# Optimization experiments

Hardware: AMD Instinct MI355X
Metric: run time of the kernel (lower is better)

Reference implementation:

```python
import jax, jax.numpy as jnp
import numpy as np

B, N_P, N_S, N_REL, N_HIS, N_INST = 2, 2000, 48, 8192, 4, 8
N = N_P + N_S
NF = 128           # nf_particle = nf_relation = nf_effect
IN_DIM = 19        # n_his*3 + attr(2) + physics(1) + action(3) + density(1)
REL_DIM = 56       # 2*19 + 2*2 + 1 + 3*4 + 1
PSTEP = 3
MOTION_CLAMP = 100.0


def _lin(key, din, dout):
    return (jax.random.normal(key, (din, dout), jnp.float32) * 0.02,
            jnp.zeros((dout,), jnp.float32))


def setup_inputs() -> dict:
    key = jax.random.key(0)
    ks = jax.random.split(key, 20)
    # one-hot receiver/sender matrices (dense stand-in for sparse edges)
    rr_idx = jax.random.randint(ks[0], (B, N_REL), 0, N)
    rs_idx = jax.random.randint(ks[1], (B, N_REL), 0, N)
    Rr = jax.nn.one_hot(rr_idx, N, dtype=jnp.float32)  # [B, n_rel, N]
    Rs = jax.nn.one_hot(rs_idx, N, dtype=jnp.float32)
    inst_idx = jax.random.randint(ks[2], (B, N_P), 0, N_INST)
    p_instance = jax.nn.one_hot(inst_idx, N_INST, dtype=jnp.float32)  # [B, n_p, n_inst]

    inp = {
        'state': jax.random.normal(ks[3], (B, N_HIS, N, 3), jnp.float32),
        'attrs': jax.random.normal(ks[4], (B, N, 2), jnp.float32),
        'Rr': Rr, 'Rs': Rs, 'p_instance': p_instance,
        'action': jax.random.normal(ks[5], (B, N, 3), jnp.float32),
        'particle_den': jax.random.uniform(ks[6], (B,), jnp.float32),
        'physics_param': jax.random.normal(ks[7], (B, 1), jnp.float32),
    }
    inp['pe_W0'], inp['pe_b0'] = _lin(ks[8], IN_DIM, NF)
    inp['pe_W1'], inp['pe_b1'] = _lin(ks[9], NF, NF)
    inp['pe_W2'], inp['pe_b2'] = _lin(ks[10], NF, NF)
    # relation encoder
    inp['re_W0'], inp['re_b0'] = _lin(ks[11], REL_DIM, NF)
    inp['re_W1'], inp['re_b1'] = _lin(ks[12], NF, NF)
    inp['re_W2'], inp['re_b2'] = _lin(ks[13], NF, NF)
    # propagators (single Linear each)
    inp['pp_W'], inp['pp_b'] = _lin(ks[14], 2 * NF, NF)
    inp['rp_W'], inp['rp_b'] = _lin(ks[15], 3 * NF, NF)
    # non-rigid predictor (Linear-ReLU-Linear-ReLU-Linear)
    inp['np_W0'], inp['np_b0'] = _lin(ks[16], NF, NF)
    inp['np_W1'], inp['np_b1'] = _lin(ks[17], NF, NF)
    inp['np_W2'], inp['np_b2'] = _lin(ks[18], NF, 3)
    return inp


def _enc(x, W0, b0, W1, b1, W2, b2):
    x = jax.nn.relu(x @ W0 + b0)
    x = jax.nn.relu(x @ W1 + b1)
    return jax.nn.relu(x @ W2 + b2)


def reference(state, attrs, Rr, Rs, p_instance, action, particle_den, physics_param,
              pe_W0, pe_b0, pe_W1, pe_b1, pe_W2, pe_b2,
              re_W0, re_b0, re_W1, re_b1, re_W2, re_b2,
              pp_W, pp_b, rp_W, rp_b,
              np_W0, np_b0, np_W1, np_b1, np_W2, np_b2):
    b, n = attrs.shape[0], attrs.shape[1]
    n_p = p_instance.shape[1]
    n_s = n - n_p
    n_inst = p_instance.shape[2]

    # temporal residuals + current state (state_normalize=False)
    state_res = state[:, 1:] - state[:, :-1]                 # [B, n_his-1, N, 3]
    state_norm = jnp.concatenate([state_res, state[:, -1:]], axis=1)
    state_norm_t = jnp.transpose(state_norm, (0, 2, 1, 3)).reshape(b, n, N_HIS * 3)

    # particle inputs: attrs | state | physics | action | density
    phys = jnp.broadcast_to(physics_param[:, None, :], (b, n_p, physics_param.shape[1]))
    phys = jnp.concatenate([phys, jnp.zeros((b, n_s, physics_param.shape[1]), state.dtype)], axis=1)
    den = jnp.broadcast_to(particle_den[:, None, None], (b, n_p, 1))
    den = jnp.concatenate([den, jnp.zeros((b, n_s, 1), state.dtype)], axis=1)
    p_inputs = jnp.concatenate([attrs, state_norm_t, phys, action, den], axis=2)  # [B,N,19]

    # relation inputs via one-hot gather (dense bmm in original)
    p_r = jnp.matmul(Rr, p_inputs)
    p_s = jnp.matmul(Rs, p_inputs)
    a_r = jnp.matmul(Rr, attrs)
    a_s = jnp.matmul(Rs, attrs)
    g = jnp.concatenate([p_instance, jnp.zeros((b, n_s, n_inst), state.dtype)], axis=1)
    group_diff = jnp.sum(jnp.abs(jnp.matmul(Rr, g) - jnp.matmul(Rs, g)), axis=2, keepdims=True)
    pos_diff = jnp.matmul(Rr, state_norm_t) - jnp.matmul(Rs, state_norm_t)
    dens_diff = jnp.matmul(Rr, den) - jnp.matmul(Rs, den)
    rel_inputs = jnp.concatenate([p_r, p_s, a_r, a_s, group_diff, pos_diff, dens_diff], axis=2)  # [B,n_rel,56]

    particle_encode = _enc(p_inputs, pe_W0, pe_b0, pe_W1, pe_b1, pe_W2, pe_b2)   # [B,N,128]
    relation_encode = _enc(rel_inputs, re_W0, re_b0, re_W1, re_b1, re_W2, re_b2)  # [B,n_rel,128]

    particle_effect = particle_encode
    for _ in range(PSTEP):
        eff_r = jnp.matmul(Rr, particle_effect)   # gather to edges
        eff_s = jnp.matmul(Rs, particle_effect)
        rel_in = jnp.concatenate([relation_encode, eff_r, eff_s], axis=2)   # [B,n_rel,384]
        effect_rel = jax.nn.relu(rel_in @ rp_W + rp_b)                      # relation propagator
        agg = jnp.einsum('brn,brd->bnd', Rr, effect_rel)                    # scatter-add (Rr_t bmm)
        p_in = jnp.concatenate([particle_encode, agg], axis=2)              # [B,N,256]
        particle_effect = jax.nn.relu(p_in @ pp_W + pp_b + particle_effect)  # residual propagator

    h = jax.nn.relu(particle_effect[:, :n_p] @ np_W0 + np_b0)
    h = jax.nn.relu(h @ np_W1 + np_b1)
    motion = h @ np_W2 + np_b2                                              # [B,n_p,3]
    motion = jnp.clip(motion, -MOTION_CLAMP, MOTION_CLAMP)
    pred_pos = state[:, -1, :n_p] + motion
    return pred_pos
```

## Files before the change

### kernel.cpp

```cpp
#include <hip/hip_runtime.h>

#define B 2
#define N_P 2000
#define N_ALL 2048
#define N_REL 8192
#define N_INST 8
#define NF 128
#define DEG_CAP 64

typedef unsigned short u16;
typedef __attribute__((ext_vector_type(8))) short bf16x8;
typedef __attribute__((ext_vector_type(4))) float f32x4;

__device__ __forceinline__ u16 f2bf(float f) {
    union { float f; unsigned u; } v; v.f = f;
    unsigned r = v.u + 0x7FFFu + ((v.u >> 16) & 1u);
    return (u16)(r >> 16);
}
__device__ __forceinline__ float bf2f(u16 h) {
    union { unsigned u; float f; } v; v.u = ((unsigned)h) << 16; return v.f;
}

#define MFMA16(a, b, c) __builtin_amdgcn_mfma_f32_16x16x32_bf16((a), (b), (c), 0, 0, 0)
#define SWZ(row, col) ((col) ^ (((row) & 7) << 3))

#define NWT 13
struct WtCvt {
    const float* src[NWT];
    int K[NWT];
    int Kpad[NWT];
    int cum[NWT + 1];
};

#define H0_SCAN_BLKS 8192
#define H0_CVT_BLKS  752
#define H0_PIN_BLKS  16
#define H0_TOTAL (H0_SCAN_BLKS + H0_CVT_BLKS + H0_PIN_BLKS)

__global__ __launch_bounds__(256) void scan_h0(
    const float* __restrict__ Rr, const float* __restrict__ Rs,
    int* __restrict__ rr, int* __restrict__ rs,
    WtCvt d, u16* __restrict__ wt, int wt_total,
    const float* __restrict__ state, const float* __restrict__ attrs,
    const float* __restrict__ action, const float* __restrict__ den,
    const float* __restrict__ phys, u16* __restrict__ P)
{
    int blk = blockIdx.x;
    if (blk < H0_SCAN_BLKS) {
        int lane = threadIdx.x & 63;
        int r = blk * 4 + (threadIdx.x >> 6);
        const float* base = (r < 16384 ? Rr + (size_t)r * N_ALL
                                       : Rs + (size_t)(r - 16384) * N_ALL);
        const f32x4* s = reinterpret_cast<const f32x4*>(base) + lane;
        f32x4 v[4];
        #pragma unroll
        for (int i = 0; i < 4; ++i) v[i] = s[64 * i];
        int f = -1;
        #pragma unroll
        for (int i = 0; i < 4; ++i) {
            int bi = (lane + 64 * i) * 4;
            if (v[i].x != 0.f) f = bi;
            if (v[i].y != 0.f) f = bi + 1;
            if (v[i].z != 0.f) f = bi + 2;
            if (v[i].w != 0.f) f = bi + 3;
        }
        #pragma unroll
        for (int off = 32; off; off >>= 1) f = max(f, __shfl_xor(f, off));
        if (lane == 0) {
            int* outp = (r < 16384) ? rr : rs;
            outp[r & 16383] = f;
        }
        return;
    }
    blk -= H0_SCAN_BLKS;
    if (blk < H0_CVT_BLKS) {
        int t = blk * 256 + threadIdx.x;
        if (t >= wt_total) return;
        int m = 0;
        while (t >= d.cum[m + 1]) m++;
        int loc = t - d.cum[m];
        int Kp = d.Kpad[m];
        int c = loc / Kp, k = loc - c * Kp;
        float v = (k < d.K[m]) ? d.src[m][(size_t)k * NF + c] : 0.f;
        wt[t] = f2bf(v);
        return;
    }
    blk -= H0_CVT_BLKS;
    {
        int t = blk * 256 + threadIdx.x;
        if (t >= B * N_ALL) return;
        int b = t >> 11, n = t & 2047;
        float o[19];
        o[0] = attrs[t * 2]; o[1] = attrs[t * 2 + 1];
        #pragma unroll
        for (int h = 0; h < 3; ++h)
            #pragma unroll
            for (int c = 0; c < 3; ++c)
                o[2 + h * 3 + c] = state[(((size_t)b * 4 + h + 1) * N_ALL + n) * 3 + c]
                                 - state[(((size_t)b * 4 + h)     * N_ALL + n) * 3 + c];
        #pragma unroll
        for (int c = 0; c < 3; ++c)
            o[11 + c] = state[(((size_t)b * 4 + 3) * N_ALL + n) * 3 + c];
        o[14] = (n < N_P) ? phys[b] : 0.f;
        #pragma unroll
        for (int c = 0; c < 3; ++c) o[15 + c] = action[t * 3 + c];
        o[18] = (n < N_P) ? den[b] : 0.f;
        u16* dst = P + (size_t)t * 32;
        #pragma unroll
        for (int k = 0; k < 19; ++k) dst[k] = f2bf(o[k]);
        #pragma unroll
        for (int k = 19; k < 32; ++k) dst[k] = 0;
    }
}

template<int START>
__global__ __launch_bounds__(256) void scan_stripe(
    const float* __restrict__ Rr, const float* __restrict__ Rs,
    int* __restrict__ rr, int* __restrict__ rs, int* __restrict__ cnt)
{
    if (blockIdx.x >= 8192) {
        int t = (blockIdx.x - 8192) * 256 + threadIdx.x;
        if (t < B * N_ALL) cnt[t] = 0;
        return;
    }
    int lane = threadIdx.x & 63;
    int r = blockIdx.x * 4 + (threadIdx.x >> 6);
    int* outp = (r < 16384) ? rr : rs;
    int e = r & 16383;
    if (outp[e] >= 0) return;
    const float* base = ((r < 16384) ? Rr + (size_t)r * N_ALL
                                     : Rs + (size_t)(r - 16384) * N_ALL) + START;
    const f32x4* s = reinterpret_cast<const f32x4*>(base + lane * 8);
    f32x4 v0 = s[0], v1 = s[1];
    int f = -1;
    int bi = START + lane * 8;
    #pragma unroll
    for (int j = 0; j < 4; ++j) {
        if (v0[j] != 0.f) f = bi + j;
        if (v1[j] != 0.f) f = bi + 4 + j;
    }
    #pragma unroll
    for (int off = 32; off; off >>= 1) f = max(f, __shfl_xor(f, off));
    if (lane == 0) outp[e] = f;
}

__device__ __forceinline__ void ldsA_gemm(const u16* T, const u16* __restrict__ wtm,
                                          f32x4 acc[8], int r16, int g4)
{
    #pragma unroll
    for (int cf = 0; cf < 8; ++cf) acc[cf] = (f32x4){0.f, 0.f, 0.f, 0.f};
    #pragma unroll
    for (int kf = 0; kf < 4; ++kf) {
        int kcol = kf * 32 + g4 * 8;
        bf16x8 a = *reinterpret_cast<const bf16x8*>(&T[r16 * NF + SWZ(r16, kcol)]);
        #pragma unroll
        for (int cf = 0; cf < 8; ++cf) {
            bf16x8 bv = *reinterpret_cast<const bf16x8*>(wtm + (size_t)(cf * 16 + r16) * NF + kcol);
            acc[cf] = MFMA16(a, bv, acc[cf]);
        }
    }
}
__device__ __forceinline__ void tile_store(u16* T, f32x4 acc[8], const float* __restrict__ bias,
                                           int r16, int g4)
{
    #pragma unroll
    for (int cf = 0; cf < 8; ++cf) {
        float bb = bias[cf * 16 + r16];
        #pragma unroll
        for (int i = 0; i < 4; ++i) {
            int row = g4 * 4 + i, col = cf * 16 + r16;
            T[row * NF + SWZ(row, col)] = f2bf(fmaxf(acc[cf][i] + bb, 0.f));
        }
    }
}

#define ENC_REL_BLKS 256
#define ENC_PART_BLKS 64
#define ENC_FILL_BLKS 8
#define ENC_TOTAL (ENC_REL_BLKS + ENC_PART_BLKS + ENC_FILL_BLKS)

__global__ __launch_bounds__(256) void enc2(
    const u16* __restrict__ P, const float* __restrict__ attrs,
    const float* __restrict__ p_inst,
    const int* __restrict__ rr, const int* __restrict__ rs,
    const u16* __restrict__ wpe0, const u16* __restrict__ wpe1, const u16* __restrict__ wpe2,
    const float* __restrict__ pb0, const float* __restrict__ pb1, const float* __restrict__ pb2,
    const u16* __restrict__ wre0, const u16* __restrict__ wre1, const u16* __restrict__ wre2,
    const float* __restrict__ rb0, const float* __restrict__ rb1, const float* __restrict__ rb2,
    const float* __restrict__ rp_b, const u16* __restrict__ wrp0t,
    const u16* __restrict__ wpp0t, const u16* __restrict__ wrp1t, const u16* __restrict__ wrp2t,
    u16* __restrict__ penc, u16* __restrict__ relencW,
    float* __restrict__ Zp, u16* __restrict__ Zrs0,
    int* __restrict__ cnt, int2* __restrict__ buckets)
{
    __shared__ __align__(16) char smem[40960];
    int tid = threadIdx.x;
    int blk = blockIdx.x;

    if (blk >= ENC_REL_BLKS + ENC_PART_BLKS) {
        int t = (blk - ENC_REL_BLKS - ENC_PART_BLKS) * 256 + tid;
        for (int e = t; e < B * N_REL; e += ENC_FILL_BLKS * 256) {
            int n = ((e >> 13) << 11) + rr[e];
            int pos = atomicAdd(&cnt[n], 1);
            if (pos < DEG_CAP) {
                int2 v; v.x = e; v.y = ((e >> 13) << 11) + rs[e];
                buckets[(size_t)n * DEG_CAP + pos] = v;
            }
        }
        return;
    }

    u16* ri = (u16*)smem;
    int w = tid >> 6, lane = tid & 63;
    int r16 = lane & 15, g4 = lane >> 4;
    u16* T0 = (u16*)(smem + 8192 + w * 8192);
    u16* T1 = T0 + 2048;
    f32x4 acc[8];

    if (blk < ENC_REL_BLKS) {
        {
            int row = tid >> 2;
            int q = tid & 3;
            int grow = blk * 64 + row;
            int b = grow >> 13;
            int ir = rr[grow], is_ = rs[grow];
            const u16* pr = P + ((size_t)(b << 11) + ir) * 32;
            const u16* ps = P + ((size_t)(b << 11) + is_) * 32;
            float gd = 0.f;
            if (q == 2) {
                #pragma unroll
                for (int k = 0; k < N_INST; ++k) {
                    float gr = (ir < N_P) ? p_inst[((size_t)b * N_P + ir) * N_INST + k] : 0.f;
                    float gs = (is_ < N_P) ? p_inst[((size_t)b * N_P + is_) * N_INST + k] : 0.f;
                    gd += fabsf(gr - gs);
                }
            }
            #pragma unroll
            for (int j = 0; j < 16; ++j) {
                int c = q * 16 + j;
                u16 hv;
                if (c < 19)       hv = pr[c];
                else if (c < 38)  hv = ps[c - 19];
                else if (c < 40)  hv = f2bf(attrs[((size_t)(b << 11) + ir) * 2 + (c - 38)]);
                else if (c < 42)  hv = f2bf(attrs[((size_t)(b << 11) + is_) * 2 + (c - 40)]);
                else if (c == 42) hv = f2bf(gd);
                else if (c < 55)  hv = f2bf(bf2f(pr[c - 41]) - bf2f(ps[c - 41]));
                else if (c == 55) hv = f2bf(bf2f(pr[18]) - bf2f(ps[18]));
                else              hv = 0;
                ri[row * 64 + SWZ(row, c)] = hv;
            }
        }
        __syncthreads();
        int rbase = blk * 64 + w * 16;
        #pragma unroll
        for (int cf = 0; cf < 8; ++cf) acc[cf] = (f32x4){0.f, 0.f, 0.f, 0.f};
        #pragma unroll
        for (int kf = 0; kf < 2; ++kf) {
            int kcol = kf * 32 + g4 * 8;
            int lr = w * 16 + r16;
            bf16x8 a = *reinterpret_cast<const bf16x8*>(&ri[lr * 64 + SWZ(lr, kcol)]);
            #pragma unroll
            for (int cf = 0; cf < 8; ++cf) {
                bf16x8 bv = *reinterpret_cast<const bf16x8*>(wre0 + (size_t)(cf * 16 + r16) * 64 + kcol);
                acc[cf] = MFMA16(a, bv, acc[cf]);
            }
        }
        tile_store(T0, acc, rb0, r16, g4);
        ldsA_gemm(T0, wre1, acc, r16, g4);
        tile_store(T1, acc, rb1, r16, g4);
        ldsA_gemm(T1, wre2, acc, r16, g4);
        tile_store(T0, acc, rb2, r16, g4);
        ldsA_gemm(T0, wrp0t, acc, r16, g4);
        #pragma unroll
        for (int cf = 0; cf < 8; ++cf) {
            float bb = rp_b[cf * 16 + r16];
            #pragma unroll
            for (int i = 0; i < 4; ++i) {
                int grow = rbase + g4 * 4 + i;
                relencW[(size_t)grow * NF + cf * 16 + r16] = f2bf(acc[cf][i] + bb);
            }
        }
        return;
    }

    int blk2 = blk - ENC_REL_BLKS;
    int rbase = blk2 * 64 + w * 16;
    #pragma unroll
    for (int cf = 0; cf < 8; ++cf) acc[cf] = (f32x4){0.f, 0.f, 0.f, 0.f};
    {
        int kcol = g4 * 8;
        bf16x8 a = *reinterpret_cast<const bf16x8*>(P + (size_t)(rbase + r16) * 32 + kcol);
        #pragma unroll
        for (int cf = 0; cf < 8; ++cf) {
            bf16x8 bv = *reinterpret_cast<const bf16x8*>(wpe0 + (size_t)(cf * 16 + r16) * 32 + kcol);
            acc[cf] = MFMA16(a, bv, acc[cf]);
        }
    }
    tile_store(T0, acc, pb0, r16, g4);
    ldsA_gemm(T0, wpe1, acc, r16, g4);
    tile_store(T1, acc, pb1, r16, g4);
    ldsA_gemm(T1, wpe2, acc, r16, g4);
    tile_store(T0, acc, pb2, r16, g4);
    #pragma unroll
    for (int cf = 0; cf < 8; ++cf)
        #pragma unroll
        for (int i = 0; i < 4; ++i) {
            int row = g4 * 4 + i, col = cf * 16 + r16;
            penc[(size_t)(rbase + row) * NF + col] = T0[row * NF + SWZ(row, col)];
        }
    ldsA_gemm(T0, wpp0t, acc, r16, g4);
    #pragma unroll
    for (int cf = 0; cf < 8; ++cf)
        #pragma unroll
        for (int i = 0; i < 4; ++i)
            Zp[(size_t)(rbase + g4 * 4 + i) * NF + cf * 16 + r16] = acc[cf][i];
    ldsA_gemm(T0, wrp1t, acc, r16, g4);
    #pragma unroll
    for (int cf = 0; cf < 8; ++cf)
        #pragma unroll
        for (int i = 0; i < 4; ++i)
            Zrs0[(size_t)(rbase + g4 * 4 + i) * 256 + cf * 16 + r16] = f2bf(acc[cf][i]);
    ldsA_gemm(T0, wrp2t, acc, r16, g4);
    #pragma unroll
    for (int cf = 0; cf < 8; ++cf)
        #pragma unroll
        for (int i = 0; i < 4; ++i)
            Zrs0[(size_t)(rbase + g4 * 4 + i) * 256 + 128 + cf * 16 + r16] = f2bf(acc[cf][i]);
}

template<int LAST>
__global__ __launch_bounds__(256) void step_c(
    const int* __restrict__ cnt, const int2* __restrict__ buckets,
    const u16* __restrict__ relencW, const u16* __restrict__ Zrs,
    const float* __restrict__ Zp, const float* __restrict__ pp_b,
    const u16* __restrict__ eff_prev,
    const u16* __restrict__ wpp1t, const u16* __restrict__ wrp1t, const u16* __restrict__ wrp2t,
    u16* __restrict__ eff_out, u16* __restrict__ Zrs_out,
    const u16* __restrict__ wnp0t, const u16* __restrict__ wnp1t,
    const float* __restrict__ nb0, const float* __restrict__ nb1,
    const float* __restrict__ np_W2, const float* __restrict__ nb2,
    const float* __restrict__ state, float* __restrict__ out)
{
    __shared__ float aggL[32][NF];
    __shared__ u16 tw[2][2][16 * NF];
    int w = threadIdx.x >> 6, lane = threadIdx.x & 63;
    int r16 = lane & 15, g4 = lane >> 4;
    int nbase = blockIdx.x * 32;

    {
        int ln = threadIdx.x >> 3;
        int q  = threadIdx.x & 7;
        int n  = nbase + ln;
        const u16* zrp = Zrs + (size_t)n * 256 + q * 16;
        bf16x8 z0 = *reinterpret_cast<const bf16x8*>(zrp);
        bf16x8 z1 = *reinterpret_cast<const bf16x8*>(zrp + 8);
        float zr[16];
        #pragma unroll
        for (int j = 0; j < 8; ++j) { zr[j] = bf2f((u16)z0[j]); zr[8 + j] = bf2f((u16)z1[j]); }
        float a16[16];
        #pragma unroll
        for (int j = 0; j < 16; ++j) a16[j] = 0.f;
        int k1 = min(cnt[n], DEG_CAP);
        const int2* eb_base = buckets + (size_t)n * DEG_CAP;
        for (int k = 0; k < k1; k += 4) {
            int m = k1 - k;
            int2 eb[4];
            #pragma unroll
            for (int t = 0; t < 4; ++t) if (t < m) eb[t] = eb_base[k + t];
            #pragma unroll
            for (int t = 0; t < 4; ++t) if (t < m) {
                const u16* rwp = relencW + (size_t)eb[t].x * NF + q * 16;
                const u16* zsp = Zrs + (size_t)eb[t].y * 256 + 128 + q * 16;
                bf16x8 rw0 = *reinterpret_cast<const bf16x8*>(rwp);
                bf16x8 rw1 = *reinterpret_cast<const bf16x8*>(rwp + 8);
                bf16x8 zs0 = *reinterpret_cast<const bf16x8*>(zsp);
                bf16x8 zs1 = *reinterpret_cast<const bf16x8*>(zsp + 8);
                #pragma unroll
                for (int j = 0; j < 8; ++j) {
                    a16[j]     += fmaxf(bf2f((u16)rw0[j]) + zr[j]     + bf2f((u16)zs0[j]), 0.f);
                    a16[8 + j] += fmaxf(bf2f((u16)rw1[j]) + zr[8 + j] + bf2f((u16)zs1[j]), 0.f);
                }
            }
        }
        int c0 = q * 16;
        int pc0 = c0 ^ ((ln & 7) << 3);
        int pc1 = (c0 + 8) ^ ((ln & 7) << 3);
        #pragma unroll
        for (int j = 0; j < 8; ++j) {
            aggL[ln][pc0 + j] = a16[j];
            aggL[ln][pc1 + j] = a16[8 + j];
        }
    }
    __syncthreads();
    if (w >= 2) return;

    u16* T0 = tw[w][0]; u16* T1 = tw[w][1];
    f32x4 acc[8];
    #pragma unroll
    for (int cf = 0; cf < 8; ++cf) acc[cf] = (f32x4){0.f, 0.f, 0.f, 0.f};
    int lrow = w * 16 + r16;
    #pragma unroll
    for (int kf = 0; kf < 4; ++kf) {
        int kcol = kf * 32 + g4 * 8;
        int pc = kcol ^ ((lrow & 7) << 3);
        float4 lo = *reinterpret_cast<const float4*>(&aggL[lrow][pc]);
        float4 hi = *reinterpret_cast<const float4*>(&aggL[lrow][pc + 4]);
        bf16x8 a;
        a[0] = (short)f2bf(lo.x); a[1] = (short)f2bf(lo.y);
        a[2] = (short)f2bf(lo.z); a[3] = (short)f2bf(lo.w);
        a[4] = (short)f2bf(hi.x); a[5] = (short)f2bf(hi.y);
        a[6] = (short)f2bf(hi.z); a[7] = (short)f2bf(hi.w);
        #pragma unroll
        for (int cf = 0; cf < 8; ++cf) {
            bf16x8 bv = *reinterpret_cast<const bf16x8*>(wpp1t + (size_t)(cf * 16 + r16) * NF + kcol);
            acc[cf] = MFMA16(a, bv, acc[cf]);
        }
    }
    int rbase = nbase + w * 16;
    #pragma unroll
    for (int cf = 0; cf < 8; ++cf) {
        int col = cf * 16 + r16;
        float bb = pp_b[col];
        #pragma unroll
        for (int i = 0; i < 4; ++i) {
            int trow = g4 * 4 + i;
            int grow = rbase + trow;
            float v = acc[cf][i] + bb + Zp[(size_t)grow * NF + col]
                    + bf2f(eff_prev[(size_t)grow * NF + col]);
            u16 hv = f2bf(fmaxf(v, 0.f));
            T0[trow * NF + SWZ(trow, col)] = hv;
            if (!LAST) eff_out[(size_t)grow * NF + col] = hv;
        }
    }
    if (!LAST) {
        ldsA_gemm(T0, wrp1t, acc, r16, g4);
        #pragma unroll
        for (int cf = 0; cf < 8; ++cf)
            #pragma unroll
            for (int i = 0; i < 4; ++i)
                Zrs_out[(size_t)(rbase + g4 * 4 + i) * 256 + cf * 16 + r16] = f2bf(acc[cf][i]);
        ldsA_gemm(T0, wrp2t, acc, r16, g4);
        #pragma unroll
        for (int cf = 0; cf < 8; ++cf)
            #pragma unroll
            for (int i = 0; i < 4; ++i)
                Zrs_out[(size_t)(rbase + g4 * 4 + i) * 256 + 128 + cf * 16 + r16] = f2bf(acc[cf][i]);
    } else {
        ldsA_gemm(T0, wnp0t, acc, r16, g4);
        tile_store(T1, acc, nb0, r16, g4);
        ldsA_gemm(T1, wnp1t, acc, r16, g4);
        tile_store(T0, acc, nb1, r16, g4);
        if (g4 < 3) {
            int grow = rbase + r16;
            int b = grow >> 11, n = grow & 2047;
            if (n < N_P) {
                float s = nb2[g4];
                for (int k = 0; k < NF; ++k)
                    s += bf2f(T0[r16 * NF + SWZ(r16, k)]) * np_W2[k * 3 + g4];
                s = fminf(fmaxf(s, -100.f), 100.f);
                out[((size_t)b * N_P + n) * 3 + g4] =
                    s + state[(((size_t)b * 4 + 3) * N_ALL + n) * 3 + g4];
            }
        }
    }
}

extern "C" void kernel_launch(void* const* d_in, const int* in_sizes, int n_in,
                              void* d_out, int out_size, void* d_ws, size_t ws_size,
                              hipStream_t stream) {
    (void)in_sizes; (void)n_in; (void)out_size; (void)ws_size;
    const float* state      = (const float*)d_in[0];
    const float* attrs      = (const float*)d_in[1];
    const float* Rr         = (const float*)d_in[2];
    const float* Rs         = (const float*)d_in[3];
    const float* p_instance = (const float*)d_in[4];
    const float* action     = (const float*)d_in[5];
    const float* den        = (const float*)d_in[6];
    const float* phys       = (const float*)d_in[7];
    const float* pe_W0 = (const float*)d_in[8];  const float* pe_b0 = (const float*)d_in[9];
    const float* pe_W1 = (const float*)d_in[10]; const float* pe_b1 = (const float*)d_in[11];
    const float* pe_W2 = (const float*)d_in[12]; const float* pe_b2 = (const float*)d_in[13];
    const float* re_W0 = (const float*)d_in[14]; const float* re_b0 = (const float*)d_in[15];
    const float* re_W1 = (const float*)d_in[16]; const float* re_b1 = (const float*)d_in[17];
    const float* re_W2 = (const float*)d_in[18]; const float* re_b2 = (const float*)d_in[19];
    const float* pp_W  = (const float*)d_in[20]; const float* pp_b  = (const float*)d_in[21];
    const float* rp_W  = (const float*)d_in[22]; const float* rp_b  = (const float*)d_in[23];
    const float* np_W0 = (const float*)d_in[24]; const float* np_b0 = (const float*)d_in[25];
    const float* np_W1 = (const float*)d_in[26]; const float* np_b1 = (const float*)d_in[27];
    const float* np_W2 = (const float*)d_in[28]; const float* np_b2 = (const float*)d_in[29];

    char* base = (char*)d_ws;
    size_t off = 0;
    auto alloc = [&](size_t bytes) -> void* {
        off = (off + 255) & ~(size_t)255;
        void* p = base + off; off += bytes; return p;
    };
    const int RN = B * N_ALL;
    const int RE = B * N_REL;
    int*   rr      = (int*)alloc(RE * 4);
    int*   rs      = (int*)alloc(RE * 4);
    int*   cnt     = (int*)alloc(RN * 4);
    int2*  buckets = (int2*)alloc((size_t)RN * DEG_CAP * 8);
    u16*   P       = (u16*)alloc((size_t)RN * 32 * 2);
    u16*   penc    = (u16*)alloc((size_t)RN * NF * 2);
    u16*   relencW = (u16*)alloc((size_t)RE * NF * 2);
    float* Zp      = (float*)alloc((size_t)RN * NF * 4);
    u16*   ZrsA    = (u16*)alloc((size_t)RN * 256 * 2);
    u16*   ZrsB    = (u16*)alloc((size_t)RN * 256 * 2);
    u16*   effX    = (u16*)alloc((size_t)RN * NF * 2);
    u16*   effY    = (u16*)alloc((size_t)RN * NF * 2);

    WtCvt d;
    const float* srcs[NWT] = {pe_W0, pe_W1, pe_W2, re_W0, re_W1, re_W2,
                              rp_W, rp_W + 128 * NF, rp_W + 256 * NF,
                              pp_W, pp_W + 128 * NF, np_W0, np_W1};
    const int Ks[NWT]  = {19, 128, 128, 56, 128, 128, 128, 128, 128, 128, 128, 128, 128};
    const int Kps[NWT] = {32, 128, 128, 64, 128, 128, 128, 128, 128, 128, 128, 128, 128};
    d.cum[0] = 0;
    for (int i = 0; i < NWT; ++i) {
        d.src[i] = srcs[i]; d.K[i] = Ks[i]; d.Kpad[i] = Kps[i];
        d.cum[i + 1] = d.cum[i] + NF * Kps[i];
    }
    int wt_total = d.cum[NWT];
    u16* wt = (u16*)alloc((size_t)wt_total * 2);
    const u16 *wpe0 = wt + d.cum[0], *wpe1 = wt + d.cum[1], *wpe2 = wt + d.cum[2];
    const u16 *wre0 = wt + d.cum[3], *wre1 = wt + d.cum[4], *wre2 = wt + d.cum[5];
    const u16 *wrp0t = wt + d.cum[6], *wrp1t = wt + d.cum[7], *wrp2t = wt + d.cum[8];
    const u16 *wpp0t = wt + d.cum[9], *wpp1t = wt + d.cum[10];
    const u16 *wnp0t = wt + d.cum[11], *wnp1t = wt + d.cum[12];

    scan_h0<<<H0_TOTAL, 256, 0, stream>>>(Rr, Rs, rr, rs, d, wt, wt_total,
                                          state, attrs, action, den, phys, P);
    scan_stripe<1024><<<8192, 256, 0, stream>>>(Rr, Rs, rr, rs, cnt);
    scan_stripe<1536><<<8192 + 16, 256, 0, stream>>>(Rr, Rs, rr, rs, cnt);

    enc2<<<ENC_TOTAL, 256, 0, stream>>>(P, attrs, p_instance, rr, rs,
        wpe0, wpe1, wpe2, pe_b0, pe_b1, pe_b2,
        wre0, wre1, wre2, re_b0, re_b1, re_b2,
        rp_b, wrp0t, wpp0t, wrp1t, wrp2t,
        penc, relencW, Zp, ZrsA, cnt, buckets);

    const u16* Zcur = ZrsA;
    const u16* effp = penc;
    u16* Znext[2] = {ZrsB, ZrsA};
    u16* effn[2]  = {effX, effY};
    for (int s = 0; s < 3; ++s) {
        if (s < 2) {
            step_c<0><<<RN / 32, 256, 0, stream>>>(cnt, buckets, relencW, Zcur,
                Zp, pp_b, effp, wpp1t, wrp1t, wrp2t, effn[s], Znext[s],
                wnp0t, wnp1t, np_b0, np_b1, np_W2, np_b2, state, (float*)d_out);
            Zcur = Znext[s];
            effp = effn[s];
        } else {
            step_c<1><<<RN / 32, 256, 0, stream>>>(cnt, buckets, relencW, Zcur,
                Zp, pp_b, effp, wpp1t, wrp1t, wrp2t, nullptr, nullptr,
                wnp0t, wnp1t, np_b0, np_b1, np_W2, np_b2, state, (float*)d_out);
        }
    }
}
```

Before: 130.5 us.

## Fuse three propagation step launches into one persistent kernel with grid barriers

The three step_c launches are replaced by a single step_m kernel of 128 blocks that runs all three propagation steps, separated by a software grid barrier built from an atomic counter. The counter is reset inside scan_stripe. The aim is to remove two kernel launch gaps and their tail effects. The risk is that the spin barrier needs all 128 blocks resident at once, which holds on this GPU; block-to-node mapping is unchanged (RN/32 = 128).

```diff
diff --git a/kernel.cpp b/kernel.cpp
--- a/kernel.cpp
+++ b/kernel.cpp
@@ -116,11 +116,13 @@
 template<int START>
 __global__ __launch_bounds__(256) void scan_stripe(
     const float* __restrict__ Rr, const float* __restrict__ Rs,
-    int* __restrict__ rr, int* __restrict__ rs, int* __restrict__ cnt)
+    int* __restrict__ rr, int* __restrict__ rs,
+    int* __restrict__ cnt, int* __restrict__ bar)
 {
     if (blockIdx.x >= 8192) {
         int t = (blockIdx.x - 8192) * 256 + threadIdx.x;
         if (t < B * N_ALL) cnt[t] = 0;
+        if (t == 0) *bar = 0;
         return;
     }
     int lane = threadIdx.x & 63;
@@ -328,21 +330,35 @@
             Zrs0[(size_t)(rbase + g4 * 4 + i) * 256 + 128 + cf * 16 + r16] = f2bf(acc[cf][i]);
 }
 
+struct StepP {
+    const int* cnt; const int2* buckets;
+    const u16* relencW; const float* Zp; const float* pp_b;
+    const u16* wpp1t; const u16* wrp1t; const u16* wrp2t;
+    const u16 *wnp0t, *wnp1t; const float *nb0, *nb1;
+    const float* np_W2; const float* nb2;
+    const float* state; float* out;
+    const u16* penc; u16 *effX, *effY, *ZrsA, *ZrsB;
+    int* bar;
+};
+
+__device__ __forceinline__ void grid_bar(int* bar, int expected)
+{
+    __syncthreads();
+    if (threadIdx.x == 0) {
+        __threadfence();
+        atomicAdd(bar, 1);
+        while (atomicAdd(bar, 0) < expected) { }
+        __threadfence();
+    }
+    __syncthreads();
+}
+
 template<int LAST>
-__global__ __launch_bounds__(256) void step_c(
-    const int* __restrict__ cnt, const int2* __restrict__ buckets,
-    const u16* __restrict__ relencW, const u16* __restrict__ Zrs,
-    const float* __restrict__ Zp, const float* __restrict__ pp_b,
-    const u16* __restrict__ eff_prev,
-    const u16* __restrict__ wpp1t, const u16* __restrict__ wrp1t, const u16* __restrict__ wrp2t,
-    u16* __restrict__ eff_out, u16* __restrict__ Zrs_out,
-    const u16* __restrict__ wnp0t, const u16* __restrict__ wnp1t,
-    const float* __restrict__ nb0, const float* __restrict__ nb1,
-    const float* __restrict__ np_W2, const float* __restrict__ nb2,
-    const float* __restrict__ state, float* __restrict__ out)
-{
-    __shared__ float aggL[32][NF];
-    __shared__ u16 tw[2][2][16 * NF];
+__device__ void step_body(const StepP& p,
+                          float (*aggL)[NF], u16* twbase,
+                          const u16* Zrs, const u16* eff_prev,
+                          u16* eff_out, u16* Zrs_out)
+{
     int w = threadIdx.x >> 6, lane = threadIdx.x & 63;
     int r16 = lane & 15, g4 = lane >> 4;
     int nbase = blockIdx.x * 32;
@@ -360,8 +376,8 @@
         float a16[16];
         #pragma unroll
         for (int j = 0; j < 16; ++j) a16[j] = 0.f;
-        int k1 = min(cnt[n], DEG_CAP);
-        const int2* eb_base = buckets + (size_t)n * DEG_CAP;
+        int k1 = min(p.cnt[n], DEG_CAP);
+        const int2* eb_base = p.buckets + (size_t)n * DEG_CAP;
         for (int k = 0; k < k1; k += 4) {
             int m = k1 - k;
             int2 eb[4];
@@ -369,7 +385,7 @@
             for (int t = 0; t < 4; ++t) if (t < m) eb[t] = eb_base[k + t];
             #pragma unroll
             for (int t = 0; t < 4; ++t) if (t < m) {
-                const u16* rwp = relencW + (size_t)eb[t].x * NF + q * 16;
+                const u16* rwp = p.relencW + (size_t)eb[t].x * NF + q * 16;
                 const u16* zsp = Zrs + (size_t)eb[t].y * 256 + 128 + q * 16;
                 bf16x8 rw0 = *reinterpret_cast<const bf16x8*>(rwp);
                 bf16x8 rw1 = *reinterpret_cast<const bf16x8*>(rwp + 8);
@@ -392,77 +408,93 @@
         }
     }
     __syncthreads();
-    if (w >= 2) return;
-
-    u16* T0 = tw[w][0]; u16* T1 = tw[w][1];
-    f32x4 acc[8];
-    #pragma unroll
-    for (int cf = 0; cf < 8; ++cf) acc[cf] = (f32x4){0.f, 0.f, 0.f, 0.f};
-    int lrow = w * 16 + r16;
-    #pragma unroll
-    for (int kf = 0; kf < 4; ++kf) {
-        int kcol = kf * 32 + g4 * 8;
-        int pc = kcol ^ ((lrow & 7) << 3);
-        float4 lo = *reinterpret_cast<const float4*>(&aggL[lrow][pc]);
-        float4 hi = *reinterpret_cast<const float4*>(&aggL[lrow][pc + 4]);
-        bf16x8 a;
-        a[0] = (short)f2bf(lo.x); a[1] = (short)f2bf(lo.y);
-        a[2] = (short)f2bf(lo.z); a[3] = (short)f2bf(lo.w);
-        a[4] = (short)f2bf(hi.x); a[5] = (short)f2bf(hi.y);
-        a[6] = (short)f2bf(hi.z); a[7] = (short)f2bf(hi.w);
+    if (w < 2) {
+        u16* T0 = twbase + w * 4096;
+        u16* T1 = T0 + 2048;
+        f32x4 acc[8];
+        #pragma unroll
+        for (int cf = 0; cf < 8; ++cf) acc[cf] = (f32x4){0.f, 0.f, 0.f, 0.f};
+        int lrow = w * 16 + r16;
+        #pragma unroll
+        for (int kf = 0; kf < 4; ++kf) {
+            int kcol = kf * 32 + g4 * 8;
+            int pc = kcol ^ ((lrow & 7) << 3);
+            float4 lo = *reinterpret_cast<const float4*>(&aggL[lrow][pc]);
+            float4 hi = *reinterpret_cast<const float4*>(&aggL[lrow][pc + 4]);
+            bf16x8 a;
+            a[0] = (short)f2bf(lo.x); a[1] = (short)f2bf(lo.y);
+            a[2] = (short)f2bf(lo.z); a[3] = (short)f2bf(lo.w);
+            a[4] = (short)f2bf(hi.x); a[5] = (short)f2bf(hi.y);
+            a[6] = (short)f2bf(hi.z); a[7] = (short)f2bf(hi.w);
+            #pragma unroll
+            for (int cf = 0; cf < 8; ++cf) {
+                bf16x8 bv = *reinterpret_cast<const bf16x8*>(p.wpp1t + (size_t)(cf * 16 + r16) * NF + kcol);
+                acc[cf] = MFMA16(a, bv, acc[cf]);
+            }
+        }
+        int rbase = nbase + w * 16;
         #pragma unroll
         for (int cf = 0; cf < 8; ++cf) {
-            bf16x8 bv = *reinterpret_cast<const bf16x8*>(wpp1t + (size_t)(cf * 16 + r16) * NF + kcol);
-            acc[cf] = MFMA16(a, bv, acc[cf]);
-        }
-    }
-    int rbase = nbase + w * 16;
-    #pragma unroll
-    for (int cf = 0; cf < 8; ++cf) {
-        int col = cf * 16 + r16;
-        float bb = pp_b[col];
-        #pragma unroll
-        for (int i = 0; i < 4; ++i) {
-            int trow = g4 * 4 + i;
-            int grow = rbase + trow;
-            float v = acc[cf][i] + bb + Zp[(size_t)grow * NF + col]
-                    + bf2f(eff_prev[(size_t)grow * NF + col]);
-            u16 hv = f2bf(fmaxf(v, 0.f));
-            T0[trow * NF + SWZ(trow, col)] = hv;
-            if (!LAST) eff_out[(size_t)grow * NF + col] = hv;
-        }
-    }
-    if (!LAST) {
-        ldsA_gemm(T0, wrp1t, acc, r16, g4);
-        #pragma unroll
-        for (int cf = 0; cf < 8; ++cf)
-            #pragma unroll
-            for (int i = 0; i < 4; ++i)
-                Zrs_out[(size_t)(rbase + g4 * 4 + i) * 256 + cf * 16 + r16] = f2bf(acc[cf][i]);
-        ldsA_gemm(T0, wrp2t, acc, r16, g4);
-        #pragma unroll
-        for (int cf = 0; cf < 8; ++cf)
-            #pragma unroll
-            for (int i = 0; i < 4; ++i)
-                Zrs_out[(size_t)(rbase + g4 * 4 + i) * 256 + 128 + cf * 16 + r16] = f2bf(acc[cf][i]);
-    } else {
-        ldsA_gemm(T0, wnp0t, acc, r16, g4);
-        tile_store(T1, acc, nb0, r16, g4);
-        ldsA_gemm(T1, wnp1t, acc, r16, g4);
-        tile_store(T0, acc, nb1, r16, g4);
-        if (g4 < 3) {
-            int grow = rbase + r16;
-            int b = grow >> 11, n = grow & 2047;
-            if (n < N_P) {
-                float s = nb2[g4];
-                for (int k = 0; k < NF; ++k)
-                    s += bf2f(T0[r16 * NF + SWZ(r16, k)]) * np_W2[k * 3 + g4];
-                s = fminf(fmaxf(s, -100.f), 100.f);
-                out[((size_t)b * N_P + n) * 3 + g4] =
-                    s + state[(((size_t)b * 4 + 3) * N_ALL + n) * 3 + g4];
-            }
-        }
-    }
+            int col = cf * 16 + r16;
+            float bb = p.pp_b[col];
+            #pragma unroll
+            for (int i = 0; i < 4; ++i) {
+                int trow = g4 * 4 + i;
+                int grow = rbase + trow;
+                float v = acc[cf][i] + bb + p.Zp[(size_t)grow * NF + col]
+                        + bf2f(eff_prev[(size_t)grow * NF + col]);
+                u16 hv = f2bf(fmaxf(v, 0.f));
+                T0[trow * NF + SWZ(trow, col)] = hv;
+                if (!LAST) eff_out[(size_t)grow * NF + col] = hv;
+            }
+        }
+        if (!LAST) {
+            f32x4 acc2[8];
+            ldsA_gemm(T0, p.wrp1t, acc2, r16, g4);
+            #pragma unroll
+            for (int cf = 0; cf < 8; ++cf)
+                #pragma unroll
+                for (int i = 0; i < 4; ++i)
+                    Zrs_out[(size_t)(rbase + g4 * 4 + i) * 256 + cf * 16 + r16] = f2bf(acc2[cf][i]);
+            ldsA_gemm(T0, p.wrp2t, acc2, r16, g4);
+            #pragma unroll
+            for (int cf = 0; cf < 8; ++cf)
+                #pragma unroll
+                for (int i = 0; i < 4; ++i)
+                    Zrs_out[(size_t)(rbase + g4 * 4 + i) * 256 + 128 + cf * 16 + r16] = f2bf(acc2[cf][i]);
+        } else {
+            f32x4 acc2[8];
+            ldsA_gemm(T0, p.wnp0t, acc2, r16, g4);
+            tile_store(T1, acc2, p.nb0, r16, g4);
+            ldsA_gemm(T1, p.wnp1t, acc2, r16, g4);
+            tile_store(T0, acc2, p.nb1, r16, g4);
+            if (g4 < 3) {
+                int grow = rbase + r16;
+                int b = grow >> 11, n = grow & 2047;
+                if (n < N_P) {
+                    float s = p.nb2[g4];
+                    for (int k = 0; k < NF; ++k)
+                        s += bf2f(T0[r16 * NF + SWZ(r16, k)]) * p.np_W2[k * 3 + g4];
+                    s = fminf(fmaxf(s, -100.f), 100.f);
+                    p.out[((size_t)b * N_P + n) * 3 + g4] =
+                        s + p.state[(((size_t)b * 4 + 3) * N_ALL + n) * 3 + g4];
+                }
+            }
+        }
+    }
+}
+
+__global__ __launch_bounds__(256) void step_m(StepP p)
+{
+    __shared__ float aggL[32][NF];
+    __shared__ u16 tw[2][2][16 * NF];
+    u16* twbase = &tw[0][0][0];
+
+    step_body<0>(p, aggL, twbase, p.ZrsA, p.penc, p.effX, p.ZrsB);
+    grid_bar(p.bar, 128);
+    step_body<0>(p, aggL, twbase, p.ZrsB, p.effX, p.effY, p.ZrsA);
+    grid_bar(p.bar, 256);
+    step_body<1>(p, aggL, twbase, p.ZrsA, p.effY, nullptr, nullptr);
 }
 
 extern "C" void kernel_launch(void* const* d_in, const int* in_sizes, int n_in,
@@ -500,6 +532,7 @@
     int*   rr      = (int*)alloc(RE * 4);
     int*   rs      = (int*)alloc(RE * 4);
     int*   cnt     = (int*)alloc(RN * 4);
+    int*   bar     = (int*)alloc(256);
     int2*  buckets = (int2*)alloc((size_t)RN * DEG_CAP * 8);
     u16*   P       = (u16*)alloc((size_t)RN * 32 * 2);
     u16*   penc    = (u16*)alloc((size_t)RN * NF * 2);
@@ -531,8 +564,8 @@
 
     scan_h0<<<H0_TOTAL, 256, 0, stream>>>(Rr, Rs, rr, rs, d, wt, wt_total,
                                           state, attrs, action, den, phys, P);
-    scan_stripe<1024><<<8192, 256, 0, stream>>>(Rr, Rs, rr, rs, cnt);
-    scan_stripe<1536><<<8192 + 16, 256, 0, stream>>>(Rr, Rs, rr, rs, cnt);
+    scan_stripe<1024><<<8192, 256, 0, stream>>>(Rr, Rs, rr, rs, cnt, bar);
+    scan_stripe<1536><<<8192 + 16, 256, 0, stream>>>(Rr, Rs, rr, rs, cnt, bar);
 
     enc2<<<ENC_TOTAL, 256, 0, stream>>>(P, attrs, p_instance, rr, rs,
         wpe0, wpe1, wpe2, pe_b0, pe_b1, pe_b2,
@@ -540,21 +573,15 @@
         rp_b, wrp0t, wpp0t, wrp1t, wrp2t,
         penc, relencW, Zp, ZrsA, cnt, buckets);
 
-    const u16* Zcur = ZrsA;
-    const u16* effp = penc;
-    u16* Znext[2] = {ZrsB, ZrsA};
-    u16* effn[2]  = {effX, effY};
-    for (int s = 0; s < 3; ++s) {
-        if (s < 2) {
-            step_c<0><<<RN / 32, 256, 0, stream>>>(cnt, buckets, relencW, Zcur,
-                Zp, pp_b, effp, wpp1t, wrp1t, wrp2t, effn[s], Znext[s],
-                wnp0t, wnp1t, np_b0, np_b1, np_W2, np_b2, state, (float*)d_out);
-            Zcur = Znext[s];
-            effp = effn[s];
-        } else {
-            step_c<1><<<RN / 32, 256, 0, stream>>>(cnt, buckets, relencW, Zcur,
-                Zp, pp_b, effp, wpp1t, wrp1t, wrp2t, nullptr, nullptr,
-                wnp0t, wnp1t, np_b0, np_b1, np_W2, np_b2, state, (float*)d_out);
-        }
-    }
-}
+    StepP sp;
+    sp.cnt = cnt; sp.buckets = buckets;
+    sp.relencW = relencW; sp.Zp = Zp; sp.pp_b = pp_b;
+    sp.wpp1t = wpp1t; sp.wrp1t = wrp1t; sp.wrp2t = wrp2t;
+    sp.wnp0t = wnp0t; sp.wnp1t = wnp1t; sp.nb0 = np_b0; sp.nb1 = np_b1;
+    sp.np_W2 = np_W2; sp.nb2 = np_b2;
+    sp.state = state; sp.out = (float*)d_out;
+    sp.penc = penc; sp.effX = effX; sp.effY = effY; sp.ZrsA = ZrsA; sp.ZrsB = ZrsB;
+    sp.bar = bar;
+
+    step_m<<<128, 256, 0, stream>>>(sp);
+}
```

Result: slower. 166.6 us (+27.7%).

## Halve per-block rows and split column work across waves in encoder and step kernels

Applied to the files above, without the earlier changes.

step_c now processes 16 nodes per 128-thread block, and both waves share the GEMMs by each computing 64 output columns, instead of half the waves exiting after aggregation. enc2 likewise moves to 128-thread blocks covering 32 rows, doubling the block count. The first Rr/Rs scan stage now covers only the first 512 columns with contiguous 8-float loads per lane, and an extra scan_stripe<512> launch covers the next 512. The aim is to raise occupancy and cut idle waves, at the cost of more blocks, extra __syncthreads, and one more kernel launch.

```diff
diff --git a/kernel.cpp b/kernel.cpp
--- a/kernel.cpp
+++ b/kernel.cpp
@@ -32,12 +32,12 @@
     int cum[NWT + 1];
 };
 
-#define H0_SCAN_BLKS 8192
-#define H0_CVT_BLKS  752
-#define H0_PIN_BLKS  16
-#define H0_TOTAL (H0_SCAN_BLKS + H0_CVT_BLKS + H0_PIN_BLKS)
-
-__global__ __launch_bounds__(256) void scan_h0(
+#define Q0_SCAN_BLKS 8192
+#define Q0_CVT_BLKS  752
+#define Q0_PIN_BLKS  16
+#define Q0_TOTAL (Q0_SCAN_BLKS + Q0_CVT_BLKS + Q0_PIN_BLKS)
+
+__global__ __launch_bounds__(256) void scan_q0(
     const float* __restrict__ Rr, const float* __restrict__ Rs,
     int* __restrict__ rr, int* __restrict__ rs,
     WtCvt d, u16* __restrict__ wt, int wt_total,
@@ -46,23 +46,19 @@
     const float* __restrict__ phys, u16* __restrict__ P)
 {
     int blk = blockIdx.x;
-    if (blk < H0_SCAN_BLKS) {
+    if (blk < Q0_SCAN_BLKS) {
         int lane = threadIdx.x & 63;
         int r = blk * 4 + (threadIdx.x >> 6);
         const float* base = (r < 16384 ? Rr + (size_t)r * N_ALL
                                        : Rs + (size_t)(r - 16384) * N_ALL);
-        const f32x4* s = reinterpret_cast<const f32x4*>(base) + lane;
-        f32x4 v[4];
-        #pragma unroll
-        for (int i = 0; i < 4; ++i) v[i] = s[64 * i];
+        const f32x4* s = reinterpret_cast<const f32x4*>(base + lane * 8);
+        f32x4 v0 = s[0], v1 = s[1];
         int f = -1;
-        #pragma unroll
-        for (int i = 0; i < 4; ++i) {
-            int bi = (lane + 64 * i) * 4;
-            if (v[i].x != 0.f) f = bi;
-            if (v[i].y != 0.f) f = bi + 1;
-            if (v[i].z != 0.f) f = bi + 2;
-            if (v[i].w != 0.f) f = bi + 3;
+        int bi = lane * 8;
+        #pragma unroll
+        for (int j = 0; j < 4; ++j) {
+            if (v0[j] != 0.f) f = bi + j;
+            if (v1[j] != 0.f) f = bi + 4 + j;
         }
         #pragma unroll
         for (int off = 32; off; off >>= 1) f = max(f, __shfl_xor(f, off));
@@ -72,8 +68,8 @@
         }
         return;
     }
-    blk -= H0_SCAN_BLKS;
-    if (blk < H0_CVT_BLKS) {
+    blk -= Q0_SCAN_BLKS;
+    if (blk < Q0_CVT_BLKS) {
         int t = blk * 256 + threadIdx.x;
         if (t >= wt_total) return;
         int m = 0;
@@ -85,7 +81,7 @@
         wt[t] = f2bf(v);
         return;
     }
-    blk -= H0_CVT_BLKS;
+    blk -= Q0_CVT_BLKS;
     {
         int t = blk * 256 + threadIdx.x;
         if (t >= B * N_ALL) return;
@@ -160,6 +156,22 @@
         }
     }
 }
+__device__ __forceinline__ void ldsA_gemm4(const u16* T, const u16* __restrict__ wtm,
+                                           int colbase, f32x4 acc[4], int r16, int g4)
+{
+    #pragma unroll
+    for (int cf = 0; cf < 4; ++cf) acc[cf] = (f32x4){0.f, 0.f, 0.f, 0.f};
+    #pragma unroll
+    for (int kf = 0; kf < 4; ++kf) {
+        int kcol = kf * 32 + g4 * 8;
+        bf16x8 a = *reinterpret_cast<const bf16x8*>(&T[r16 * NF + SWZ(r16, kcol)]);
+        #pragma unroll
+        for (int cf = 0; cf < 4; ++cf) {
+            bf16x8 bv = *reinterpret_cast<const bf16x8*>(wtm + (size_t)(colbase + cf * 16 + r16) * NF + kcol);
+            acc[cf] = MFMA16(a, bv, acc[cf]);
+        }
+    }
+}
 __device__ __forceinline__ void tile_store(u16* T, f32x4 acc[8], const float* __restrict__ bias,
                                            int r16, int g4)
 {
@@ -174,12 +186,12 @@
     }
 }
 
-#define ENC_REL_BLKS 256
-#define ENC_PART_BLKS 64
+#define ENC_REL_BLKS 512
+#define ENC_PART_BLKS 128
 #define ENC_FILL_BLKS 8
 #define ENC_TOTAL (ENC_REL_BLKS + ENC_PART_BLKS + ENC_FILL_BLKS)
 
-__global__ __launch_bounds__(256) void enc2(
+__global__ __launch_bounds__(128) void enc2(
     const u16* __restrict__ P, const float* __restrict__ attrs,
     const float* __restrict__ p_inst,
     const int* __restrict__ rr, const int* __restrict__ rs,
@@ -193,13 +205,14 @@
     float* __restrict__ Zp, u16* __restrict__ Zrs0,
     int* __restrict__ cnt, int2* __restrict__ buckets)
 {
-    __shared__ __align__(16) char smem[40960];
+    __shared__ u16 ri[32 * 64];
+    __shared__ u16 tw[2][2][16 * NF];
     int tid = threadIdx.x;
     int blk = blockIdx.x;
 
     if (blk >= ENC_REL_BLKS + ENC_PART_BLKS) {
-        int t = (blk - ENC_REL_BLKS - ENC_PART_BLKS) * 256 + tid;
-        for (int e = t; e < B * N_REL; e += ENC_FILL_BLKS * 256) {
+        int t = (blk - ENC_REL_BLKS - ENC_PART_BLKS) * 128 + tid;
+        for (int e = t; e < B * N_REL; e += ENC_FILL_BLKS * 128) {
             int n = ((e >> 13) << 11) + rr[e];
             int pos = atomicAdd(&cnt[n], 1);
             if (pos < DEG_CAP) {
@@ -210,18 +223,17 @@
         return;
     }
 
-    u16* ri = (u16*)smem;
     int w = tid >> 6, lane = tid & 63;
     int r16 = lane & 15, g4 = lane >> 4;
-    u16* T0 = (u16*)(smem + 8192 + w * 8192);
-    u16* T1 = T0 + 2048;
+    u16* T0 = tw[w][0];
+    u16* T1 = tw[w][1];
     f32x4 acc[8];
 
     if (blk < ENC_REL_BLKS) {
         {
             int row = tid >> 2;
             int q = tid & 3;
-            int grow = blk * 64 + row;
+            int grow = blk * 32 + row;
             int b = grow >> 13;
             int ir = rr[grow], is_ = rs[grow];
             const u16* pr = P + ((size_t)(b << 11) + ir) * 32;
@@ -251,7 +263,7 @@
             }
         }
         __syncthreads();
-        int rbase = blk * 64 + w * 16;
+        int rbase = blk * 32 + w * 16;
         #pragma unroll
         for (int cf = 0; cf < 8; ++cf) acc[cf] = (f32x4){0.f, 0.f, 0.f, 0.f};
         #pragma unroll
@@ -284,7 +296,7 @@
     }
 
     int blk2 = blk - ENC_REL_BLKS;
-    int rbase = blk2 * 64 + w * 16;
+    int rbase = blk2 * 32 + w * 16;
     #pragma unroll
     for (int cf = 0; cf < 8; ++cf) acc[cf] = (f32x4){0.f, 0.f, 0.f, 0.f};
     {
@@ -329,7 +341,7 @@
 }
 
 template<int LAST>
-__global__ __launch_bounds__(256) void step_c(
+__global__ __launch_bounds__(128) void step_c(
     const int* __restrict__ cnt, const int2* __restrict__ buckets,
     const u16* __restrict__ relencW, const u16* __restrict__ Zrs,
     const float* __restrict__ Zp, const float* __restrict__ pp_b,
@@ -341,15 +353,17 @@
     const float* __restrict__ np_W2, const float* __restrict__ nb2,
     const float* __restrict__ state, float* __restrict__ out)
 {
-    __shared__ float aggL[32][NF];
-    __shared__ u16 tw[2][2][16 * NF];
-    int w = threadIdx.x >> 6, lane = threadIdx.x & 63;
+    __shared__ float aggL[16][NF];
+    __shared__ u16 T0s[16 * NF];
+    __shared__ u16 T1s[16 * NF];
+    int tid = threadIdx.x;
+    int w = tid >> 6, lane = tid & 63;
     int r16 = lane & 15, g4 = lane >> 4;
-    int nbase = blockIdx.x * 32;
+    int nbase = blockIdx.x * 16;
 
     {
-        int ln = threadIdx.x >> 3;
-        int q  = threadIdx.x & 7;
+        int ln = tid >> 3;
+        int q  = tid & 7;
         int n  = nbase + ln;
         const u16* zrp = Zrs + (size_t)n * 256 + q * 16;
         bf16x8 z0 = *reinterpret_cast<const bf16x8*>(zrp);
@@ -392,71 +406,90 @@
         }
     }
     __syncthreads();
-    if (w >= 2) return;
-
-    u16* T0 = tw[w][0]; u16* T1 = tw[w][1];
-    f32x4 acc[8];
-    #pragma unroll
-    for (int cf = 0; cf < 8; ++cf) acc[cf] = (f32x4){0.f, 0.f, 0.f, 0.f};
-    int lrow = w * 16 + r16;
+
+    int cb = w * 64;
+    f32x4 acc[4];
+    #pragma unroll
+    for (int cf = 0; cf < 4; ++cf) acc[cf] = (f32x4){0.f, 0.f, 0.f, 0.f};
     #pragma unroll
     for (int kf = 0; kf < 4; ++kf) {
         int kcol = kf * 32 + g4 * 8;
-        int pc = kcol ^ ((lrow & 7) << 3);
-        float4 lo = *reinterpret_cast<const float4*>(&aggL[lrow][pc]);
-        float4 hi = *reinterpret_cast<const float4*>(&aggL[lrow][pc + 4]);
+        int pc = kcol ^ ((r16 & 7) << 3);
+        float4 lo = *reinterpret_cast<const float4*>(&aggL[r16][pc]);
+        float4 hi = *reinterpret_cast<const float4*>(&aggL[r16][pc + 4]);
         bf16x8 a;
         a[0] = (short)f2bf(lo.x); a[1] = (short)f2bf(lo.y);
         a[2] = (short)f2bf(lo.z); a[3] = (short)f2bf(lo.w);
         a[4] = (short)f2bf(hi.x); a[5] = (short)f2bf(hi.y);
         a[6] = (short)f2bf(hi.z); a[7] = (short)f2bf(hi.w);
         #pragma unroll
-        for (int cf = 0; cf < 8; ++cf) {
-            bf16x8 bv = *reinterpret_cast<const bf16x8*>(wpp1t + (size_t)(cf * 16 + r16) * NF + kcol);
+        for (int cf = 0; cf < 4; ++cf) {
+            bf16x8 bv = *reinterpret_cast<const bf16x8*>(wpp1t + (size_t)(cb + cf * 16 + r16) * NF + kcol);
             acc[cf] = MFMA16(a, bv, acc[cf]);
         }
     }
-    int rbase = nbase + w * 16;
-    #pragma unroll
-    for (int cf = 0; cf < 8; ++cf) {
-        int col = cf * 16 + r16;
+    #pragma unroll
+    for (int cf = 0; cf < 4; ++cf) {
+        int col = cb + cf * 16 + r16;
         float bb = pp_b[col];
         #pragma unroll
         for (int i = 0; i < 4; ++i) {
             int trow = g4 * 4 + i;
-            int grow = rbase + trow;
+            int grow = nbase + trow;
             float v = acc[cf][i] + bb + Zp[(size_t)grow * NF + col]
                     + bf2f(eff_prev[(size_t)grow * NF + col]);
             u16 hv = f2bf(fmaxf(v, 0.f));
-            T0[trow * NF + SWZ(trow, col)] = hv;
+            T0s[trow * NF + SWZ(trow, col)] = hv;
             if (!LAST) eff_out[(size_t)grow * NF + col] = hv;
         }
     }
+    __syncthreads();
+
     if (!LAST) {
-        ldsA_gemm(T0, wrp1t, acc, r16, g4);
-        #pragma unroll
-        for (int cf = 0; cf < 8; ++cf)
+        f32x4 a2[4];
+        ldsA_gemm4(T0s, wrp1t, cb, a2, r16, g4);
+        #pragma unroll
+        for (int cf = 0; cf < 4; ++cf)
             #pragma unroll
             for (int i = 0; i < 4; ++i)
-                Zrs_out[(size_t)(rbase + g4 * 4 + i) * 256 + cf * 16 + r16] = f2bf(acc[cf][i]);
-        ldsA_gemm(T0, wrp2t, acc, r16, g4);
-        #pragma unroll
-        for (int cf = 0; cf < 8; ++cf)
+                Zrs_out[(size_t)(nbase + g4 * 4 + i) * 256 + cb + cf * 16 + r16] = f2bf(a2[cf][i]);
+        ldsA_gemm4(T0s, wrp2t, cb, a2, r16, g4);
+        #pragma unroll
+        for (int cf = 0; cf < 4; ++cf)
             #pragma unroll
             for (int i = 0; i < 4; ++i)
-                Zrs_out[(size_t)(rbase + g4 * 4 + i) * 256 + 128 + cf * 16 + r16] = f2bf(acc[cf][i]);
+                Zrs_out[(size_t)(nbase + g4 * 4 + i) * 256 + 128 + cb + cf * 16 + r16] = f2bf(a2[cf][i]);
     } else {
-        ldsA_gemm(T0, wnp0t, acc, r16, g4);
-        tile_store(T1, acc, nb0, r16, g4);
-        ldsA_gemm(T1, wnp1t, acc, r16, g4);
-        tile_store(T0, acc, nb1, r16, g4);
-        if (g4 < 3) {
-            int grow = rbase + r16;
+        f32x4 a2[4];
+        ldsA_gemm4(T0s, wnp0t, cb, a2, r16, g4);
+        #pragma unroll
+        for (int cf = 0; cf < 4; ++cf) {
+            float bb = nb0[cb + cf * 16 + r16];
+            #pragma unroll
+            for (int i = 0; i < 4; ++i) {
+                int row = g4 * 4 + i, col = cb + cf * 16 + r16;
+                T1s[row * NF + SWZ(row, col)] = f2bf(fmaxf(a2[cf][i] + bb, 0.f));
+            }
+        }
+        __syncthreads();
+        ldsA_gemm4(T1s, wnp1t, cb, a2, r16, g4);
+        #pragma unroll
+        for (int cf = 0; cf < 4; ++cf) {
+            float bb = nb1[cb + cf * 16 + r16];
+            #pragma unroll
+            for (int i = 0; i < 4; ++i) {
+                int row = g4 * 4 + i, col = cb + cf * 16 + r16;
+                T0s[row * NF + SWZ(row, col)] = f2bf(fmaxf(a2[cf][i] + bb, 0.f));
+            }
+        }
+        __syncthreads();
+        if (w == 0 && g4 < 3) {
+            int grow = nbase + r16;
             int b = grow >> 11, n = grow & 2047;
             if (n < N_P) {
                 float s = nb2[g4];
                 for (int k = 0; k < NF; ++k)
-                    s += bf2f(T0[r16 * NF + SWZ(r16, k)]) * np_W2[k * 3 + g4];
+                    s += bf2f(T0s[r16 * NF + SWZ(r16, k)]) * np_W2[k * 3 + g4];
                 s = fminf(fmaxf(s, -100.f), 100.f);
                 out[((size_t)b * N_P + n) * 3 + g4] =
                     s + state[(((size_t)b * 4 + 3) * N_ALL + n) * 3 + g4];
@@ -529,12 +562,13 @@
     const u16 *wpp0t = wt + d.cum[9], *wpp1t = wt + d.cum[10];
     const u16 *wnp0t = wt + d.cum[11], *wnp1t = wt + d.cum[12];
 
-    scan_h0<<<H0_TOTAL, 256, 0, stream>>>(Rr, Rs, rr, rs, d, wt, wt_total,
+    scan_q0<<<Q0_TOTAL, 256, 0, stream>>>(Rr, Rs, rr, rs, d, wt, wt_total,
                                           state, attrs, action, den, phys, P);
+    scan_stripe<512><<<8192, 256, 0, stream>>>(Rr, Rs, rr, rs, cnt);
     scan_stripe<1024><<<8192, 256, 0, stream>>>(Rr, Rs, rr, rs, cnt);
     scan_stripe<1536><<<8192 + 16, 256, 0, stream>>>(Rr, Rs, rr, rs, cnt);
 
-    enc2<<<ENC_TOTAL, 256, 0, stream>>>(P, attrs, p_instance, rr, rs,
+    enc2<<<ENC_TOTAL, 128, 0, stream>>>(P, attrs, p_instance, rr, rs,
         wpe0, wpe1, wpe2, pe_b0, pe_b1, pe_b2,
         wre0, wre1, wre2, re_b0, re_b1, re_b2,
         rp_b, wrp0t, wpp0t, wrp1t, wrp2t,
@@ -546,13 +580,13 @@
     u16* effn[2]  = {effX, effY};
     for (int s = 0; s < 3; ++s) {
         if (s < 2) {
-            step_c<0><<<RN / 32, 256, 0, stream>>>(cnt, buckets, relencW, Zcur,
+            step_c<0><<<RN / 16, 128, 0, stream>>>(cnt, buckets, relencW, Zcur,
                 Zp, pp_b, effp, wpp1t, wrp1t, wrp2t, effn[s], Znext[s],
                 wnp0t, wnp1t, np_b0, np_b1, np_W2, np_b2, state, (float*)d_out);
             Zcur = Znext[s];
             effp = effn[s];
         } else {
-            step_c<1><<<RN / 32, 256, 0, stream>>>(cnt, buckets, relencW, Zcur,
+            step_c<1><<<RN / 16, 128, 0, stream>>>(cnt, buckets, relencW, Zcur,
                 Zp, pp_b, effp, wpp1t, wrp1t, wrp2t, nullptr, nullptr,
                 wnp0t, wnp1t, np_b0, np_b1, np_W2, np_b2, state, (float*)d_out);
         }
```

After: 113.2 us. 1.15x faster.
